# Optimization experiments

Measured on AMD Instinct MI355X. Metric: run time of the kernel, lower is better.

## Reference

```python
import jax, jax.numpy as jnp
import numpy as np

N, E, G = 50000, 1600000, 64
IN, HID, OUT = 128, 64, 64
NEG_SLOPE = 0.2


def _p(key, shape):
    return jax.random.normal(key, shape, dtype=jnp.float32) * 0.1


def setup_inputs() -> dict:
    key = jax.random.key(0)
    ks = jax.random.split(key, 24)
    inp = {
        "x": jax.random.normal(ks[0], (N, IN), dtype=jnp.float32),
        "edge_index": jax.random.randint(ks[1], (2, E), 0, N),
        "edge_attr": jax.random.uniform(ks[2], (E, 1), dtype=jnp.float32),
        "batch": jnp.sort(jax.random.randint(ks[3], (N,), 0, G)),
        # GATv2 layer 1 (in=128 -> 64, heads=1)
        "Wl1": _p(ks[4], (IN, HID)), "bl1": _p(ks[5], (HID,)),
        "Wr1": _p(ks[6], (IN, HID)), "br1": _p(ks[7], (HID,)),
        "We1": _p(ks[8], (1, HID)), "att1": _p(ks[9], (HID,)), "bias1": _p(ks[10], (HID,)),
        # GATv2 layer 2 (64 -> 64)
        "Wl2": _p(ks[11], (HID, OUT)), "bl2": _p(ks[12], (OUT,)),
        "Wr2": _p(ks[13], (HID, OUT)), "br2": _p(ks[14], (OUT,)),
        "We2": _p(ks[15], (1, OUT)), "att2": _p(ks[16], (OUT,)), "bias2": _p(ks[17], (OUT,)),
        # MLP head: fc1 (64->32), bn1 (32), fc3 (32->1)
        "W_fc1": _p(ks[18], (OUT, OUT // 2)), "b_fc1": _p(ks[19], (OUT // 2,)),
        "bn_gamma": jnp.ones((OUT // 2,), jnp.float32),
        "bn_beta": jnp.zeros((OUT // 2,), jnp.float32),
        "bn_mean": _p(ks[20], (OUT // 2,)),
        "bn_var": jax.random.uniform(ks[21], (OUT // 2,), jnp.float32, 0.5, 1.5),
        "W_fc3": _p(ks[22], (OUT // 2, 1)), "b_fc3": _p(ks[23], (1,)),
    }
    return inp


def _add_self_loops(src, dst, edge_attr, n):
    # PyG add_self_loops with fill_value='mean': loop attr = mean of incoming edge attrs per node
    s = jax.ops.segment_sum(edge_attr, dst, num_segments=n)  # (N,1)
    c = jax.ops.segment_sum(jnp.ones((edge_attr.shape[0], 1), edge_attr.dtype), dst, num_segments=n)
    loop_attr = s / jnp.maximum(c, 1.0)
    loops = jnp.arange(n)
    return (jnp.concatenate([src, loops]), jnp.concatenate([dst, loops]),
            jnp.concatenate([edge_attr, loop_attr], axis=0))


def _gatv2(h, src, dst, e_attr, Wl, bl, Wr, br, We, att, bias, n):
    xl = h @ Wl + bl                     # (N, C) source transform
    xr = h @ Wr + br                     # (N, C) target transform
    ef = e_attr @ We                     # (E', C)
    s = jax.nn.leaky_relu(xl[src] + xr[dst] + ef, NEG_SLOPE)  # (E', C)
    logits = s @ att                     # (E',)
    m = jax.ops.segment_max(logits, dst, num_segments=n)
    m = jnp.where(jnp.isfinite(m), m, 0.0)
    p = jnp.exp(logits - m[dst])
    denom = jax.ops.segment_sum(p, dst, num_segments=n)
    alpha = p / (denom[dst] + 1e-16)
    out = jax.ops.segment_sum(alpha[:, None] * xl[src], dst, num_segments=n)
    return out + bias


def reference(x, edge_index, edge_attr, batch,
              Wl1, bl1, Wr1, br1, We1, att1, bias1,
              Wl2, bl2, Wr2, br2, We2, att2, bias2,
              W_fc1, b_fc1, bn_gamma, bn_beta, bn_mean, bn_var, W_fc3, b_fc3):
    n = x.shape[0]
    src, dst, ea = _add_self_loops(edge_index[0], edge_index[1], edge_attr, n)
    h = jax.nn.elu(_gatv2(x, src, dst, ea, Wl1, bl1, Wr1, br1, We1, att1, bias1, n))
    h = jax.nn.elu(_gatv2(h, src, dst, ea, Wl2, bl2, Wr2, br2, We2, att2, bias2, n))
    # global_mean_pool
    sums = jax.ops.segment_sum(h, batch, num_segments=G)
    cnts = jax.ops.segment_sum(jnp.ones((n, 1), h.dtype), batch, num_segments=G)
    pooled = sums / jnp.maximum(cnts, 1.0)
    # head: bn1(relu(fc1(.))) with eval-mode BN, dropout off, then fc3
    z = jax.nn.relu(pooled @ W_fc1 + b_fc1)
    z = (z - bn_mean) / jnp.sqrt(bn_var + 1e-5) * bn_gamma + bn_beta
    return z @ W_fc3 + b_fc3
```

## Files before the change

kernel.cpp:

```cpp
#include <hip/hip_runtime.h>
#include <hip/hip_fp16.h>
#include <math.h>

typedef unsigned long long u64;
typedef __attribute__((ext_vector_type(2))) _Float16 half2v;
typedef __attribute__((ext_vector_type(4))) _Float16 half4v;
typedef __attribute__((ext_vector_type(8))) _Float16 half8;
typedef __attribute__((ext_vector_type(4))) float f32x4;
typedef __attribute__((ext_vector_type(2))) float f32x2;


#define BKT     256
#define CAP     12032
#define MAXSPAN 13056
#define PEPB    4096
#define NPWP    64

__global__ void k_prep_w(const float* __restrict__ Wl1, const float* __restrict__ bl1,
                         const float* __restrict__ Wr1, const float* __restrict__ br1,
                         const float* __restrict__ Wl2, const float* __restrict__ bl2,
                         const float* __restrict__ Wr2, const float* __restrict__ br2,
                         _Float16* __restrict__ Wt1, float* __restrict__ bv1,
                         _Float16* __restrict__ Wt2, float* __restrict__ bv2, int ld1) {
    int t = blockIdx.x * blockDim.x + threadIdx.x;
    int stride = gridDim.x * blockDim.x;
    int IN1 = 1 << ld1;
    for (int i = t; i < 128 * IN1; i += stride) {
        int n = i >> ld1, k = i & (IN1 - 1);
        float v = (n < 64) ? Wl1[k * 64 + n] : Wr1[k * 64 + (n - 64)];
        Wt1[n * IN1 + k] = (_Float16)v;
    }
    for (int i = t; i < 128 * 64; i += stride) {
        int n = i >> 6, k = i & 63;
        float v = (n < 64) ? Wl2[k * 64 + n] : Wr2[k * 64 + (n - 64)];
        Wt2[n * 64 + k] = (_Float16)v;
    }
    if (t < 128) {
        bv1[t] = (t < 64) ? bl1[t] : br1[t - 64];
        bv2[t] = (t < 64) ? bl2[t] : br2[t - 64];
    }
}

template<int IN>
__device__ __forceinline__ void xf_block_mfma(
        const float* __restrict__ h,
        const _Float16* __restrict__ Wt,
        const float* __restrict__ bv,
        __half* __restrict__ xl, __half* __restrict__ xr,
        int N, int node0, _Float16* rows, int t) {
    constexpr int LDK = IN + 8;
    constexpr int Q = IN / 4;
    for (int idx = t; idx < 64 * Q; idx += 256) {
        int nn = idx / Q;
        int kk = (idx % Q) * 4;
        int node = node0 + nn;
        float4 v = {0.f, 0.f, 0.f, 0.f};
        if (node < N) v = *(const float4*)(h + (size_t)node * IN + kk);
        half4v hv = {(_Float16)v.x, (_Float16)v.y, (_Float16)v.z, (_Float16)v.w};
        *(half4v*)(rows + nn * LDK + kk) = hv;
    }
    __syncthreads();
    int lane = t & 63, w = t >> 6;
    int n0w = w * 32;
    int lr = lane & 15, lq = lane >> 4;
    f32x4 acc[4][2];
#pragma unroll
    for (int i = 0; i < 4; ++i)
#pragma unroll
        for (int j = 0; j < 2; ++j) acc[i][j] = {0.f, 0.f, 0.f, 0.f};
    const _Float16* arow = rows + lr * LDK + lq * 8;
    const _Float16* brow = Wt + (size_t)(n0w + lr) * IN + lq * 8;
#pragma unroll
    for (int k0 = 0; k0 < IN; k0 += 32) {
        half8 a0 = *(const half8*)(arow + k0);
        half8 a1 = *(const half8*)(arow + 16 * LDK + k0);
        half8 a2 = *(const half8*)(arow + 32 * LDK + k0);
        half8 a3 = *(const half8*)(arow + 48 * LDK + k0);
        half8 b0 = *(const half8*)(brow + k0);
        half8 b1 = *(const half8*)(brow + 16 * IN + k0);
        acc[0][0] = __builtin_amdgcn_mfma_f32_16x16x32_f16(a0, b0, acc[0][0], 0, 0, 0);
        acc[1][0] = __builtin_amdgcn_mfma_f32_16x16x32_f16(a1, b0, acc[1][0], 0, 0, 0);
        acc[2][0] = __builtin_amdgcn_mfma_f32_16x16x32_f16(a2, b0, acc[2][0], 0, 0, 0);
        acc[3][0] = __builtin_amdgcn_mfma_f32_16x16x32_f16(a3, b0, acc[3][0], 0, 0, 0);
        acc[0][1] = __builtin_amdgcn_mfma_f32_16x16x32_f16(a0, b1, acc[0][1], 0, 0, 0);
        acc[1][1] = __builtin_amdgcn_mfma_f32_16x16x32_f16(a1, b1, acc[1][1], 0, 0, 0);
        acc[2][1] = __builtin_amdgcn_mfma_f32_16x16x32_f16(a2, b1, acc[2][1], 0, 0, 0);
        acc[3][1] = __builtin_amdgcn_mfma_f32_16x16x32_f16(a3, b1, acc[3][1], 0, 0, 0);
    }
    float bia0 = bv[n0w + lr];
    float bia1 = bv[n0w + 16 + lr];
#pragma unroll
    for (int ni = 0; ni < 2; ++ni) {
        int dim = n0w + ni * 16 + lr;
        __half* dst = (dim < 64) ? xl : xr;
        int dd = dim & 63;
        float bb = ni ? bia1 : bia0;
#pragma unroll
        for (int mi = 0; mi < 4; ++mi) {
#pragma unroll
            for (int r = 0; r < 4; ++r) {
                int node = node0 + mi * 16 + lq * 4 + r;
                if (node < N)
                    dst[((size_t)node << 6) + dd] = __float2half(acc[mi][ni][r] + bb);
            }
        }
    }
}

union XfPartSmem {
    _Float16 rows[64 * 136];
    struct { int lh[256]; int lbase[256]; int lcur[256]; } p;
};

template<int IN>
__global__ void k_xf1_part(
        const float* __restrict__ h,
        const _Float16* __restrict__ Wt, const float* __restrict__ bv,
        __half* __restrict__ xl, __half* __restrict__ xr, int N, int nbXF,
        const int* __restrict__ ei, const float* __restrict__ ea,
        int* __restrict__ qtail, u64* __restrict__ queue, int E) {
    __shared__ XfPartSmem sm;
    int t = threadIdx.x;
    if (blockIdx.x < nbXF) {
        xf_block_mfma<IN>(h, Wt, bv, xl, xr, N, blockIdx.x * 64, sm.rows, t);
    } else {
        int pb = blockIdx.x - nbXF;
        sm.p.lh[t] = 0; sm.p.lcur[t] = 0;
        __syncthreads();
        int base = pb * PEPB;
        int end = base + PEPB; if (end > E) end = E;
        for (int e = base + t; e < end; e += 256) {
            int d = ei[E + e];
            atomicAdd(&sm.p.lh[d >> 8], 1);
        }
        __syncthreads();
        if (sm.p.lh[t]) sm.p.lbase[t] = atomicAdd(&qtail[t], sm.p.lh[t]);
        __syncthreads();
        for (int e = base + t; e < end; e += 256) {
            int d = ei[E + e];
            int src = ei[e];
            float a = ea[e];
            int b = d >> 8;
            int idx = atomicAdd(&sm.p.lcur[b], 1);
            unsigned aq = (unsigned)(a * 16777216.0f);
            queue[(size_t)b * CAP + sm.p.lbase[b] + idx] =
                (((u64)aq) << 25) | (((u64)(d & 255)) << 17) | (unsigned)src;
        }
    }
}

__device__ __forceinline__ unsigned attr_q15(float a) {
    unsigned short hb = __builtin_bit_cast(unsigned short, (_Float16)a);
    return (unsigned)(hb >> 1);
}

__global__ void __launch_bounds__(1024)
k_build(const u64* __restrict__ queue, const int* __restrict__ qtail,
        u64* __restrict__ rs2, unsigned* __restrict__ csr, int N) {
    __shared__ u64 stat[BKT];
    __shared__ int fill[BKT], sc[BKT];
    __shared__ unsigned lcsr[MAXSPAN];
    int t = threadIdx.x, b = blockIdx.x;
    if (t < BKT) stat[t] = 0;
    __syncthreads();
    int cnt = qtail[b];
    size_t q0 = (size_t)b * CAP;
    for (int i = t; i < cnt; i += 1024) {
        u64 r = queue[q0 + i];
        int dl = (int)((r >> 17) & (BKT - 1));
        atomicAdd(&stat[dl], (1ULL << 32) | (unsigned)(r >> 25));
    }
    __syncthreads();
    int dg = b * BKT + t;
    u64 p = (t < BKT) ? stat[t] : 0;
    int deg = (int)(p >> 32);
    int v = (t < BKT && dg < N) ? ((deg + 1 + 3) & ~3) : 0;
    if (t < BKT) sc[t] = v;
    __syncthreads();
    for (int off = 1; off < BKT; off <<= 1) {
        int a = (t >= off && t < BKT) ? sc[t - off] : 0;
        __syncthreads();
        if (t < BKT) sc[t] += a;
        __syncthreads();
    }
    int c0 = b * MAXSPAN;
    if (t < BKT && dg < N) {
        int basel = sc[t] - v;
        rs2[dg] = (u64)(unsigned)(c0 + basel) | (((u64)(unsigned)(c0 + basel + deg + 1)) << 32);
        fill[t] = basel;
        float mean = ((float)(unsigned)p * (1.0f / 16777216.0f)) / fmaxf((float)deg, 1.0f);
        if (basel + deg < MAXSPAN) lcsr[basel + deg] = (attr_q15(mean) << 17) | (unsigned)dg;
    }
    __syncthreads();
    for (int i = t; i < cnt; i += 1024) {
        u64 r = queue[q0 + i];
        int dl = (int)((r >> 17) & (BKT - 1));
        int pos = atomicAdd(&fill[dl], 1);
        float av = (float)(unsigned)(r >> 25) * (1.0f / 16777216.0f);
        if (pos < MAXSPAN) lcsr[pos] = (attr_q15(av) << 17) | (unsigned)(r & 0x1FFFFu);
    }
    __syncthreads();
    int span = sc[BKT - 1];
    if (span > MAXSPAN) span = MAXSPAN;
    for (int j = t; j < span; j += 1024) csr[c0 + j] = lcsr[j];
}

__global__ void k_node_xf(const float* __restrict__ h,
                          const _Float16* __restrict__ Wt, const float* __restrict__ bv,
                          __half* __restrict__ xl, __half* __restrict__ xr, int N) {
    __shared__ _Float16 rows[64 * 72];
    xf_block_mfma<64>(h, Wt, bv, xl, xr, N, blockIdx.x * 64, rows, threadIdx.x);
}

template<int CTRL>
__device__ __forceinline__ float dpp_add(float c) {
    int t = __builtin_amdgcn_update_dpp(0, __builtin_bit_cast(int, c),
                                        CTRL, 0xF, 0xF, true);
    return c + __builtin_bit_cast(float, t);
}

#define EDGE_GROUP(r, xh, cc)                                                  \
    {                                                                          \
        _Float16 ah = __builtin_bit_cast(_Float16, (unsigned short)((r >> 16) & 0xFFFEu)); \
        half2v aa = {ah, ah};                                                  \
        half2v x01 = {xh.x, xh.y}, x23 = {xh.z, xh.w};                         \
        half2v v01 = aa * We01 + (x01 + xr01);                                 \
        half2v v23 = aa * We23 + (x23 + xr23);                                 \
        half2v s01 = __builtin_elementwise_max(v01, v01 * k02);                \
        half2v s23 = __builtin_elementwise_max(v23, v23 * k02);                \
        cc = __builtin_amdgcn_fdot2(s01, at01, 0.f, false);                    \
        cc = __builtin_amdgcn_fdot2(s23, at23, cc, false);                     \
    }

__global__ void k_attn(const __half* __restrict__ xl, const __half* __restrict__ xr,
                       const unsigned* __restrict__ csr, const u64* __restrict__ rs2,
                       const float* __restrict__ We, const float* __restrict__ att,
                       const float* __restrict__ bias,
                       float* __restrict__ hout, int N) {
    int lane = threadIdx.x & 63;
    int d = (int)(((size_t)blockIdx.x * blockDim.x + threadIdx.x) >> 6);
    if (d >= N) return;
    int eq = lane >> 4;
    int fl = lane & 15;
    const float LOG2E = 1.44269504088896340736f;
    float4 Wef  = *(const float4*)(We + fl * 4);
    float4 attf = *(const float4*)(att + fl * 4);
    half2v We01 = {(_Float16)Wef.x, (_Float16)Wef.y};
    half2v We23 = {(_Float16)Wef.z, (_Float16)Wef.w};
    half2v at01 = {(_Float16)(attf.x * LOG2E), (_Float16)(attf.y * LOG2E)};
    half2v at23 = {(_Float16)(attf.z * LOG2E), (_Float16)(attf.w * LOG2E)};
    unsigned flo = (unsigned)fl * 4u;
    half4v xrh = *(const half4v*)(xr + (((unsigned)d << 6) | flo));
    half2v xr01 = {xrh.x, xrh.y}, xr23 = {xrh.z, xrh.w};
    const half2v k02 = {(_Float16)0.2f, (_Float16)0.2f};
    u64 rr = rs2[d];
    int e0 = __builtin_amdgcn_readfirstlane((int)(unsigned)rr);
    int e1 = __builtin_amdgcn_readfirstlane((int)(unsigned)(rr >> 32));
    float l = 0.f;
    f32x2 Oa = {0.f, 0.f}, Ob = {0.f, 0.f};
    int e = e0;
    for (; e + 16 <= e1; e += 16) {
        uint4 rv = *(const uint4*)(csr + e + (eq << 2));
        unsigned oA = ((rv.x & 0x1FFFFu) << 6) | flo;
        unsigned oB = ((rv.y & 0x1FFFFu) << 6) | flo;
        unsigned oC = ((rv.z & 0x1FFFFu) << 6) | flo;
        unsigned oD = ((rv.w & 0x1FFFFu) << 6) | flo;
        half4v xA = *(const half4v*)(xl + oA);
        half4v xB = *(const half4v*)(xl + oB);
        half4v xC = *(const half4v*)(xl + oC);
        half4v xD = *(const half4v*)(xl + oD);
        float cA, cB, cC, cD;
        EDGE_GROUP(rv.x, xA, cA);
        EDGE_GROUP(rv.y, xB, cB);
        EDGE_GROUP(rv.z, xC, cC);
        EDGE_GROUP(rv.w, xD, cD);
        cA = dpp_add<0xB1>(cA);  cB = dpp_add<0xB1>(cB);
        cC = dpp_add<0xB1>(cC);  cD = dpp_add<0xB1>(cD);
        cA = dpp_add<0x4E>(cA);  cB = dpp_add<0x4E>(cB);
        cC = dpp_add<0x4E>(cC);  cD = dpp_add<0x4E>(cD);
        cA = dpp_add<0x141>(cA); cB = dpp_add<0x141>(cB);
        cC = dpp_add<0x141>(cC); cD = dpp_add<0x141>(cD);
        cA = dpp_add<0x140>(cA); cB = dpp_add<0x140>(cB);
        cC = dpp_add<0x140>(cC); cD = dpp_add<0x140>(cD);
        float qA = __builtin_exp2f(cA), qB = __builtin_exp2f(cB);
        float qC = __builtin_exp2f(cC), qD = __builtin_exp2f(cD);
        l += (qA + qB) + (qC + qD);
        f32x2 qA2 = {qA, qA}, qB2 = {qB, qB}, qC2 = {qC, qC}, qD2 = {qD, qD};
        f32x2 xa01 = {(float)xA.x, (float)xA.y}, xa23 = {(float)xA.z, (float)xA.w};
        f32x2 xb01 = {(float)xB.x, (float)xB.y}, xb23 = {(float)xB.z, (float)xB.w};
        f32x2 xc01 = {(float)xC.x, (float)xC.y}, xc23 = {(float)xC.z, (float)xC.w};
        f32x2 xd01 = {(float)xD.x, (float)xD.y}, xd23 = {(float)xD.z, (float)xD.w};
        Oa = __builtin_elementwise_fma(qA2, xa01, Oa);
        Oa = __builtin_elementwise_fma(qB2, xb01, Oa);
        Oa = __builtin_elementwise_fma(qC2, xc01, Oa);
        Oa = __builtin_elementwise_fma(qD2, xd01, Oa);
        Ob = __builtin_elementwise_fma(qA2, xa23, Ob);
        Ob = __builtin_elementwise_fma(qB2, xb23, Ob);
        Ob = __builtin_elementwise_fma(qC2, xc23, Ob);
        Ob = __builtin_elementwise_fma(qD2, xd23, Ob);
    }
    for (; e < e1; e += 4) {
        int ee = e + eq;
        bool valid = ee < e1;
        unsigned r = csr[valid ? ee : (e1 - 1)];
        half4v xh = *(const half4v*)(xl + (((r & 0x1FFFFu) << 6) | flo));
        float c;
        EDGE_GROUP(r, xh, c);
        c = dpp_add<0xB1>(c);
        c = dpp_add<0x4E>(c);
        c = dpp_add<0x141>(c);
        c = dpp_add<0x140>(c);
        float q = valid ? __builtin_exp2f(c) : 0.f;
        l += q;
        Oa.x = fmaf(q, (float)xh.x, Oa.x);
        Oa.y = fmaf(q, (float)xh.y, Oa.y);
        Ob.x = fmaf(q, (float)xh.z, Ob.x);
        Ob.y = fmaf(q, (float)xh.w, Ob.y);
    }
#pragma unroll
    for (int mm = 16; mm <= 32; mm <<= 1) {
        l    += __shfl_xor(l, mm, 64);
        Oa.x += __shfl_xor(Oa.x, mm, 64);
        Oa.y += __shfl_xor(Oa.y, mm, 64);
        Ob.x += __shfl_xor(Ob.x, mm, 64);
        Ob.y += __shfl_xor(Ob.y, mm, 64);
    }
    if (eq == 0) {
        float inv = 1.0f / (l + 1e-16f);
        float4 b4 = *(const float4*)(bias + fl * 4);
        float4 res;
        res.x = fmaf(Oa.x, inv, b4.x);
        res.y = fmaf(Oa.y, inv, b4.y);
        res.z = fmaf(Ob.x, inv, b4.z);
        res.w = fmaf(Ob.y, inv, b4.w);
        res.x = res.x > 0.f ? res.x : __expf(res.x) - 1.f;
        res.y = res.y > 0.f ? res.y : __expf(res.y) - 1.f;
        res.z = res.z > 0.f ? res.z : __expf(res.z) - 1.f;
        res.w = res.w > 0.f ? res.w : __expf(res.w) - 1.f;
        *(float4*)(hout + ((size_t)d << 6) + fl * 4) = res;
    }
}

__global__ void k_pool_head(const float* __restrict__ h, const int* __restrict__ batch,
                            float* __restrict__ pooled, float* __restrict__ gcnt,
                            int N, int* __restrict__ done,
                            const float* __restrict__ W1, const float* __restrict__ b1,
                            const float* __restrict__ gam, const float* __restrict__ bet,
                            const float* __restrict__ mu, const float* __restrict__ var,
                            const float* __restrict__ W3, const float* __restrict__ b3,
                            float* __restrict__ out, int G) {
    int tid = threadIdx.x;
    int lane = tid & 63;
    int wave = (int)(((size_t)blockIdx.x * blockDim.x + tid) >> 6);
    int begin = wave * NPWP;
    if (begin < N) {
        int bidx = begin + lane;
        int bval = batch[bidx < N ? bidx : (N - 1)];
        float hv[NPWP];
#pragma unroll
        for (int j = 0; j < NPWP; ++j) {
            int n = begin + j;
            hv[j] = (n < N) ? h[((size_t)n << 6) + lane] : 0.f;
        }
        int g = __shfl(bval, 0, 64);
        float acc = 0.f, cnt = 0.f;
#pragma unroll
        for (int j = 0; j < NPWP; ++j) {
            if (begin + j < N) {
                int gn = __shfl(bval, j, 64);
                if (gn != g) {
                    atomicAdd(&pooled[((size_t)g << 6) + lane], acc);
                    if (lane == 0) atomicAdd(&gcnt[g], cnt);
                    g = gn; acc = 0.f; cnt = 0.f;
                }
                acc += hv[j];
                cnt += 1.f;
            }
        }
        atomicAdd(&pooled[((size_t)g << 6) + lane], acc);
        if (lane == 0) atomicAdd(&gcnt[g], cnt);
    }
    __threadfence();
    __syncthreads();
    __shared__ int lastFlag;
    if (tid == 0) lastFlag = (atomicAdd(done, 1) == (int)gridDim.x - 1);
    __syncthreads();
    if (lastFlag && tid < G) {
        __threadfence();
        int g = tid;
        float inv = 1.0f / fmaxf(gcnt[g], 1.0f);
        float pr[64];
        for (int k = 0; k < 64; ++k) pr[k] = pooled[((size_t)g << 6) + k] * inv;
        float o = b3[0];
        for (int j = 0; j < 32; ++j) {
            float z = b1[j];
            for (int k = 0; k < 64; ++k) z += pr[k] * W1[k * 32 + j];
            z = fmaxf(z, 0.f);
            z = (z - mu[j]) / sqrtf(var[j] + 1e-5f) * gam[j] + bet[j];
            o += z * W3[j];
        }
        out[g] = o;
    }
}

extern "C" void kernel_launch(void* const* d_in, const int* in_sizes, int n_in,
                              void* d_out, int out_size, void* d_ws, size_t ws_size,
                              hipStream_t stream) {
    const float* x    = (const float*)d_in[0];
    const int*   ei   = (const int*)d_in[1];
    const float* ea   = (const float*)d_in[2];
    const int*   batch= (const int*)d_in[3];
    const float* Wl1  = (const float*)d_in[4];
    const float* bl1  = (const float*)d_in[5];
    const float* Wr1  = (const float*)d_in[6];
    const float* br1  = (const float*)d_in[7];
    const float* We1  = (const float*)d_in[8];
    const float* att1 = (const float*)d_in[9];
    const float* bi1  = (const float*)d_in[10];
    const float* Wl2  = (const float*)d_in[11];
    const float* bl2  = (const float*)d_in[12];
    const float* Wr2  = (const float*)d_in[13];
    const float* br2  = (const float*)d_in[14];
    const float* We2  = (const float*)d_in[15];
    const float* att2 = (const float*)d_in[16];
    const float* bi2  = (const float*)d_in[17];
    const float* Wf1  = (const float*)d_in[18];
    const float* bf1  = (const float*)d_in[19];
    const float* gam  = (const float*)d_in[20];
    const float* bet  = (const float*)d_in[21];
    const float* mu   = (const float*)d_in[22];
    const float* var  = (const float*)d_in[23];
    const float* Wf3  = (const float*)d_in[24];
    const float* bf3  = (const float*)d_in[25];

    const int N    = in_sizes[3];
    const int E    = in_sizes[2];
    const int INd  = in_sizes[0] / N;
    const int ld1  = (INd == 128) ? 7 : 6;
    const int G    = out_size;
    const int NB   = (N + BKT - 1) / BKT;

    char* w = (char*)d_ws;
    auto carve = [&](size_t bytes) { char* p = w; w += (bytes + 255) & ~(size_t)255; return p; };
    __half*   xl       = (__half*)  carve((size_t)N * 64 * 2);
    __half*   xr       = (__half*)  carve((size_t)N * 64 * 2);
    float*    hbuf     = (float*)   carve((size_t)N * 64 * 4);
    unsigned* csr      = (unsigned*)carve((size_t)NB * MAXSPAN * 4);
    u64*      queue    = (u64*)     carve((size_t)NB * CAP * 8);
    u64*      rs2      = (u64*)     carve((size_t)N * 8);
    int*      qtail    = (int*)     carve((size_t)(NB + 1) * 4);
    float*    pooled   = (float*)   carve((size_t)G * 64 * 4);
    float*    gcnt     = (float*)   carve((size_t)G * 4);
    int*      done     = (int*)     carve(256);
    _Float16* Wt1      = (_Float16*)carve((size_t)128 * 128 * 2);
    float*    bv1      = (float*)   carve(128 * 4);
    _Float16* Wt2      = (_Float16*)carve((size_t)128 * 64 * 2);
    float*    bv2      = (float*)   carve(128 * 4);

    const int TB = 256;
    const int nbXF = (N + 63) / 64;
    const int attnBlocks = (N + 3) / 4;
    const int nbPart = (E + PEPB - 1) / PEPB;

    hipMemsetAsync(qtail, 0, (size_t)(NB + 1) * 4, stream);
    size_t poolRegion = (((size_t)G * 64 * 4 + 255) & ~(size_t)255)
                      + (((size_t)G * 4 + 255) & ~(size_t)255) + 256;
    hipMemsetAsync(pooled, 0, poolRegion, stream);

    k_prep_w<<<32, TB, 0, stream>>>(Wl1, bl1, Wr1, br1, Wl2, bl2, Wr2, br2,
                                    Wt1, bv1, Wt2, bv2, ld1);

    if (INd == 128)
        k_xf1_part<128><<<nbXF + nbPart, TB, 0, stream>>>(x, Wt1, bv1, xl, xr, N, nbXF,
                                                          ei, ea, qtail, queue, E);
    else
        k_xf1_part<64><<<nbXF + nbPart, TB, 0, stream>>>(x, Wt1, bv1, xl, xr, N, nbXF,
                                                         ei, ea, qtail, queue, E);
    k_build<<<NB, 1024, 0, stream>>>(queue, qtail, rs2, csr, N);

    k_attn<<<attnBlocks, TB, 0, stream>>>(xl, xr, csr, rs2, We1, att1, bi1, hbuf, N);

    k_node_xf<<<nbXF, TB, 0, stream>>>(hbuf, Wt2, bv2, xl, xr, N);
    k_attn<<<attnBlocks, TB, 0, stream>>>(xl, xr, csr, rs2, We2, att2, bi2, hbuf, N);

    const int poolWaves = (N + NPWP - 1) / NPWP;
    k_pool_head<<<(poolWaves * 64 + TB - 1) / TB, TB, 0, stream>>>(
        hbuf, batch, pooled, gcnt, N, done,
        Wf1, bf1, gam, bet, mu, var, Wf3, bf3, (float*)d_out, G);
}
```

Before: 304.1 us.

## Replace bucketed queue CSR build with global count, scan, and atomic scatter

Edge-to-CSR construction no longer goes through a two-pass bucketed queue and a per-bucket LDS build kernel. Instead, per-node degree and attribute sums are accumulated with global 64-bit atomics, a block scan with an atomic tail assigns CSR offsets, and a scatter kernel places edges using per-node atomic fill counters. This drops the queue buffer and the fixed bucket capacity limits and shortens the CSR layout. In exchange it uses many more contended global atomics, writes scattered CSR entries, and makes edge order within a row nondeterministic.

```diff
diff --git a/kernel.cpp b/kernel.cpp
--- a/kernel.cpp
+++ b/kernel.cpp
@@ -10,10 +10,8 @@
 typedef __attribute__((ext_vector_type(2))) float f32x2;
 
 
-#define BKT     256
-#define CAP     12032
-#define MAXSPAN 13056
 #define PEPB    4096
+#define PEPS    2048
 #define NPWP    64
 
 __global__ void k_prep_w(const float* __restrict__ Wl1, const float* __restrict__ bl1,
@@ -107,44 +105,26 @@
     }
 }
 
-union XfPartSmem {
-    _Float16 rows[64 * 136];
-    struct { int lh[256]; int lbase[256]; int lcur[256]; } p;
-};
-
 template<int IN>
-__global__ void k_xf1_part(
+__global__ void k_xf1_cnt(
         const float* __restrict__ h,
         const _Float16* __restrict__ Wt, const float* __restrict__ bv,
         __half* __restrict__ xl, __half* __restrict__ xr, int N, int nbXF,
         const int* __restrict__ ei, const float* __restrict__ ea,
-        int* __restrict__ qtail, u64* __restrict__ queue, int E) {
-    __shared__ XfPartSmem sm;
+        u64* __restrict__ cnt64, int E) {
+    __shared__ _Float16 rows[64 * 136];
     int t = threadIdx.x;
     if (blockIdx.x < nbXF) {
-        xf_block_mfma<IN>(h, Wt, bv, xl, xr, N, blockIdx.x * 64, sm.rows, t);
+        xf_block_mfma<IN>(h, Wt, bv, xl, xr, N, blockIdx.x * 64, rows, t);
     } else {
         int pb = blockIdx.x - nbXF;
-        sm.p.lh[t] = 0; sm.p.lcur[t] = 0;
-        __syncthreads();
         int base = pb * PEPB;
         int end = base + PEPB; if (end > E) end = E;
         for (int e = base + t; e < end; e += 256) {
             int d = ei[E + e];
-            atomicAdd(&sm.p.lh[d >> 8], 1);
-        }
-        __syncthreads();
-        if (sm.p.lh[t]) sm.p.lbase[t] = atomicAdd(&qtail[t], sm.p.lh[t]);
-        __syncthreads();
-        for (int e = base + t; e < end; e += 256) {
-            int d = ei[E + e];
-            int src = ei[e];
             float a = ea[e];
-            int b = d >> 8;
-            int idx = atomicAdd(&sm.p.lcur[b], 1);
             unsigned aq = (unsigned)(a * 16777216.0f);
-            queue[(size_t)b * CAP + sm.p.lbase[b] + idx] =
-                (((u64)aq) << 25) | (((u64)(d & 255)) << 17) | (unsigned)src;
+            atomicAdd(&cnt64[d], (1ULL << 32) | aq);
         }
     }
 }
@@ -154,55 +134,48 @@
     return (unsigned)(hb >> 1);
 }
 
-__global__ void __launch_bounds__(1024)
-k_build(const u64* __restrict__ queue, const int* __restrict__ qtail,
-        u64* __restrict__ rs2, unsigned* __restrict__ csr, int N) {
-    __shared__ u64 stat[BKT];
-    __shared__ int fill[BKT], sc[BKT];
-    __shared__ unsigned lcsr[MAXSPAN];
+__global__ void k_scan(const u64* __restrict__ cnt64, u64* __restrict__ rs2,
+                       int* __restrict__ fill, unsigned* __restrict__ csr,
+                       int* __restrict__ tail, int N) {
+    __shared__ int sc[256];
+    __shared__ int baseSh;
     int t = threadIdx.x, b = blockIdx.x;
-    if (t < BKT) stat[t] = 0;
+    int dg = b * 256 + t;
+    u64 p = (dg < N) ? cnt64[dg] : 0;
+    int deg = (int)(p >> 32);
+    int span = (dg < N) ? ((deg + 1 + 3) & ~3) : 0;
+    sc[t] = span;
     __syncthreads();
-    int cnt = qtail[b];
-    size_t q0 = (size_t)b * CAP;
-    for (int i = t; i < cnt; i += 1024) {
-        u64 r = queue[q0 + i];
-        int dl = (int)((r >> 17) & (BKT - 1));
-        atomicAdd(&stat[dl], (1ULL << 32) | (unsigned)(r >> 25));
-    }
+    for (int off = 1; off < 256; off <<= 1) {
+        int a = (t >= off) ? sc[t - off] : 0;
+        __syncthreads();
+        sc[t] += a;
+        __syncthreads();
+    }
+    if (t == 255) baseSh = atomicAdd(tail, sc[255]);
     __syncthreads();
-    int dg = b * BKT + t;
-    u64 p = (t < BKT) ? stat[t] : 0;
-    int deg = (int)(p >> 32);
-    int v = (t < BKT && dg < N) ? ((deg + 1 + 3) & ~3) : 0;
-    if (t < BKT) sc[t] = v;
-    __syncthreads();
-    for (int off = 1; off < BKT; off <<= 1) {
-        int a = (t >= off && t < BKT) ? sc[t - off] : 0;
-        __syncthreads();
-        if (t < BKT) sc[t] += a;
-        __syncthreads();
-    }
-    int c0 = b * MAXSPAN;
-    if (t < BKT && dg < N) {
-        int basel = sc[t] - v;
-        rs2[dg] = (u64)(unsigned)(c0 + basel) | (((u64)(unsigned)(c0 + basel + deg + 1)) << 32);
-        fill[t] = basel;
+    int base = baseSh + sc[t] - span;
+    if (dg < N) {
+        rs2[dg] = (u64)(unsigned)base | (((u64)(unsigned)(base + deg + 1)) << 32);
+        fill[dg] = base;
         float mean = ((float)(unsigned)p * (1.0f / 16777216.0f)) / fmaxf((float)deg, 1.0f);
-        if (basel + deg < MAXSPAN) lcsr[basel + deg] = (attr_q15(mean) << 17) | (unsigned)dg;
-    }
-    __syncthreads();
-    for (int i = t; i < cnt; i += 1024) {
-        u64 r = queue[q0 + i];
-        int dl = (int)((r >> 17) & (BKT - 1));
-        int pos = atomicAdd(&fill[dl], 1);
-        float av = (float)(unsigned)(r >> 25) * (1.0f / 16777216.0f);
-        if (pos < MAXSPAN) lcsr[pos] = (attr_q15(av) << 17) | (unsigned)(r & 0x1FFFFu);
-    }
-    __syncthreads();
-    int span = sc[BKT - 1];
-    if (span > MAXSPAN) span = MAXSPAN;
-    for (int j = t; j < span; j += 1024) csr[c0 + j] = lcsr[j];
+        csr[base + deg] = (attr_q15(mean) << 17) | (unsigned)dg;
+    }
+}
+
+__global__ void k_scatter(const int* __restrict__ ei, const float* __restrict__ ea,
+                          int* __restrict__ fill, unsigned* __restrict__ csr, int E) {
+    int t = threadIdx.x;
+    int base = blockIdx.x * PEPS;
+    int end = base + PEPS; if (end > E) end = E;
+#pragma unroll 4
+    for (int e = base + t; e < end; e += 256) {
+        int d = ei[E + e];
+        int src = ei[e];
+        float a = ea[e];
+        int pos = atomicAdd(&fill[d], 1);
+        csr[pos] = (attr_q15(a) << 17) | (unsigned)src;
+    }
 }
 
 __global__ void k_node_xf(const float* __restrict__ h,
@@ -438,17 +411,17 @@
     const int INd  = in_sizes[0] / N;
     const int ld1  = (INd == 128) ? 7 : 6;
     const int G    = out_size;
-    const int NB   = (N + BKT - 1) / BKT;
 
     char* w = (char*)d_ws;
     auto carve = [&](size_t bytes) { char* p = w; w += (bytes + 255) & ~(size_t)255; return p; };
     __half*   xl       = (__half*)  carve((size_t)N * 64 * 2);
     __half*   xr       = (__half*)  carve((size_t)N * 64 * 2);
     float*    hbuf     = (float*)   carve((size_t)N * 64 * 4);
-    unsigned* csr      = (unsigned*)carve((size_t)NB * MAXSPAN * 4);
-    u64*      queue    = (u64*)     carve((size_t)NB * CAP * 8);
+    unsigned* csr      = (unsigned*)carve((size_t)(E + 4 * N + 256) * 4);
     u64*      rs2      = (u64*)     carve((size_t)N * 8);
-    int*      qtail    = (int*)     carve((size_t)(NB + 1) * 4);
+    int*      fill     = (int*)     carve((size_t)N * 4);
+    u64*      cnt64    = (u64*)     carve((size_t)N * 8);
+    int*      tail     = (int*)     carve(256);
     float*    pooled   = (float*)   carve((size_t)G * 64 * 4);
     float*    gcnt     = (float*)   carve((size_t)G * 4);
     int*      done     = (int*)     carve(256);
@@ -458,11 +431,14 @@
     float*    bv2      = (float*)   carve(128 * 4);
 
     const int TB = 256;
-    const int nbXF = (N + 63) / 64;
+    const int nbXF   = (N + 63) / 64;
     const int attnBlocks = (N + 3) / 4;
-    const int nbPart = (E + PEPB - 1) / PEPB;
-
-    hipMemsetAsync(qtail, 0, (size_t)(NB + 1) * 4, stream);
+    const int nbCnt  = (E + PEPB - 1) / PEPB;
+    const int nbScat = (E + PEPS - 1) / PEPS;
+    const int nbScan = (N + 255) / 256;
+
+    size_t cntRegion = (((size_t)N * 8 + 255) & ~(size_t)255) + 256;
+    hipMemsetAsync(cnt64, 0, cntRegion, stream);
     size_t poolRegion = (((size_t)G * 64 * 4 + 255) & ~(size_t)255)
                       + (((size_t)G * 4 + 255) & ~(size_t)255) + 256;
     hipMemsetAsync(pooled, 0, poolRegion, stream);
@@ -471,12 +447,14 @@
                                     Wt1, bv1, Wt2, bv2, ld1);
 
     if (INd == 128)
-        k_xf1_part<128><<<nbXF + nbPart, TB, 0, stream>>>(x, Wt1, bv1, xl, xr, N, nbXF,
-                                                          ei, ea, qtail, queue, E);
+        k_xf1_cnt<128><<<nbXF + nbCnt, TB, 0, stream>>>(x, Wt1, bv1, xl, xr, N, nbXF,
+                                                        ei, ea, cnt64, E);
     else
-        k_xf1_part<64><<<nbXF + nbPart, TB, 0, stream>>>(x, Wt1, bv1, xl, xr, N, nbXF,
-                                                         ei, ea, qtail, queue, E);
-    k_build<<<NB, 1024, 0, stream>>>(queue, qtail, rs2, csr, N);
+        k_xf1_cnt<64><<<nbXF + nbCnt, TB, 0, stream>>>(x, Wt1, bv1, xl, xr, N, nbXF,
+                                                       ei, ea, cnt64, E);
+
+    k_scan<<<nbScan, TB, 0, stream>>>(cnt64, rs2, fill, csr, tail, N);
+    k_scatter<<<nbScat, TB, 0, stream>>>(ei, ea, fill, csr, E);
 
     k_attn<<<attnBlocks, TB, 0, stream>>>(xl, xr, csr, rs2, We1, att1, bi1, hbuf, N);
 
```

After: 474.3 us. 56.0% more time.
